# Optimization experiments

Hardware: AMD Instinct MI355X
Metric: run time of the kernel (lower is better)

The kernel has to match this reference:

```python
import jax, jax.numpy as jnp
import numpy as np

B = 131072
# join branch layer dims: 203 -> 175 -> 150 -> 128 -> 80 -> 48
DIMS = [203, 175, 150, 128, 80, 48]

def setup_inputs() -> dict:
    key = jax.random.key(0)
    ks = jax.random.split(key, 11)
    inp = {"x": jax.random.normal(ks[0], (B, DIMS[0]), dtype=jnp.float32)}
    for i in range(5):
        fan_in, fan_out = DIMS[i], DIMS[i + 1]
        bound = 1.0 / np.sqrt(fan_in)
        inp[f"W{i+1}"] = jax.random.uniform(ks[1 + 2 * i], (fan_out, fan_in), minval=-bound, maxval=bound, dtype=jnp.float32)
        inp[f"b{i+1}"] = jax.random.uniform(ks[2 + 2 * i], (fan_out,), minval=-bound, maxval=bound, dtype=jnp.float32)
    return inp

def reference(x, W1, b1, W2, b2, W3, b3, W4, b4, W5, b5):
    # join branch of NodeEmbedding, dropout in eval mode (identity).
    h = jnp.tanh(x @ W1.T + b1)      # [B,175]
    h = jnp.tanh(h @ W2.T + b2)      # [B,150]
    h = jnp.tanh(h @ W3.T + b3)      # [B,128]
    h = jnp.tanh(h @ W4.T + b4)      # [B,80]
    return h @ W5.T + b5             # [B,48], no activation on last layer
```

## Files before the change

kernel.cpp:

```cpp
#include <hip/hip_runtime.h>


typedef short short8 __attribute__((ext_vector_type(8)));
typedef float f32x16 __attribute__((ext_vector_type(16)));
typedef unsigned int uint;
typedef unsigned short ushort;

#define PSTR 116
#define PSTRU (PSTR*2)
#define NTHREADS 384

__device__ __forceinline__ ushort f2bf(float f) {
    uint u = __float_as_uint(f);
    u += 0x7FFFu + ((u >> 16) & 1u);
    return (ushort)(u >> 16);
}
__device__ __forceinline__ float bf2f(ushort h) { return __uint_as_float(((uint)h) << 16); }
__device__ __forceinline__ float fast_tanh(float x) {
    float e = __expf(2.0f * x);
    return 1.0f - 2.0f / (e + 1.0f);
}
__device__ __forceinline__ uint rbf(float v) {
    uint u = __float_as_uint(v);
    return u + 0x7FFFu + ((u >> 16) & 1u);
}

union U4S8 { uint4 u; short8 s; };

__global__ void prep_weights(const float* __restrict__ W1, const float* __restrict__ W2,
                             const float* __restrict__ W3, const float* __restrict__ W4,
                             const float* __restrict__ W5, char* __restrict__ ws)
{
    const int b = blockIdx.x, l = threadIdx.x;
    int layer, local;
    if      (b <  78) { layer = 0; local = b; }
    else if (b < 133) { layer = 1; local = b - 78; }
    else if (b < 173) { layer = 2; local = b - 133; }
    else if (b < 197) { layer = 3; local = b - 173; }
    else              { layer = 4; local = b - 197; }
    const int NTa[5]  = {6, 5, 4, 3, 2};
    const int FINa[5] = {203, 175, 150, 128, 80};
    const int FOa[5]  = {175, 150, 128, 80, 48};
    const float* Wp = (layer == 0) ? W1 : (layer == 1) ? W2 : (layer == 2) ? W3
                    : (layer == 3) ? W4 : W5;
    const int nt = NTa[layer], fin = FINa[layer], fout = FOa[layer];
    const int c = local / nt, t = local % nt;
    const int n  = t * 32 + (l & 31);
    const int kb = c * 16 + (l >> 5) * 8;
    uint hw[4], lw[4];
#pragma unroll
    for (int j = 0; j < 8; ++j) {
        int k = kb + j;
        float v = (n < fout && k < fin) ? Wp[(size_t)n * fin + k] : 0.0f;
        ushort hh = f2bf(v);
        ushort ll = f2bf(v - bf2f(hh));
        if (j & 1) { hw[j >> 1] |= ((uint)hh) << 16; lw[j >> 1] |= ((uint)ll) << 16; }
        else       { hw[j >> 1]  = hh;               lw[j >> 1]  = ll; }
    }
    char* dst = ws + (size_t)b * 2048 + l * 16;
    *(uint4*)dst          = make_uint4(hw[0], hw[1], hw[2], hw[3]);
    *(uint4*)(dst + 1024) = make_uint4(lw[0], lw[1], lw[2], lw[3]);
}

template<int KC, int NT, int FOUT, int PADN, bool ACT, bool LAST>
__device__ __forceinline__ void run_layer(const char* __restrict__ wsL,
    const float* __restrict__ bias, uint* aH, uint* aL, float* outg,
    int row0, int l, int w, int lx, int lh, int tid)
{
    f32x16 acc;
    {
        float bv = 0.0f;
        if (w < NT) { int n = w * 32 + lx; bv = (n < FOUT) ? bias[n] : 0.0f; }
#pragma unroll
        for (int r = 0; r < 16; ++r) acc[r] = bv;
    }

    if (w < NT) {
        const char* ha = (const char*)aH + lx * (PSTR * 4) + lh * 16;
        const char* la = (const char*)aL + lx * (PSTR * 4) + lh * 16;
#pragma unroll
        for (int c = 0; c < KC; ++c) {
            const uint4* wp = (const uint4*)wsL + (size_t)((c * NT + w) * 2) * 64 + l;
            U4S8 bh, bl, ah, al;
            bh.u = wp[0];
            bl.u = wp[64];
            ah.u = *(const uint4*)(ha + c * 32);
            al.u = *(const uint4*)(la + c * 32);
            acc = __builtin_amdgcn_mfma_f32_32x32x16_bf16(ah.s, bh.s, acc, 0, 0, 0);
            acc = __builtin_amdgcn_mfma_f32_32x32x16_bf16(al.s, bh.s, acc, 0, 0, 0);
            acc = __builtin_amdgcn_mfma_f32_32x32x16_bf16(ah.s, bl.s, acc, 0, 0, 0);
        }
    }
    if (!LAST) __syncthreads();

    if (w < NT) {
        ushort* pH = (ushort*)aH;
        ushort* pL = (ushort*)aL;
#pragma unroll
        for (int r = 0; r < 16; ++r) {
            float vv = acc[r];
            if (ACT) vv = fast_tanh(vv);
            int rowl = (r & 3) + 8 * (r >> 2) + 4 * lh;
            int col  = w * 32 + lx;
            if (LAST) {
                if (col < 48) outg[(size_t)(row0 + rowl) * 48 + col] = vv;
            } else if (col < FOUT) {
                uint r1  = rbf(vv);
                uint hib = r1 & 0xFFFF0000u;
                float lo = vv - __uint_as_float(hib);
                uint r2  = rbf(lo);
                pH[rowl * PSTRU + col] = (ushort)(r1 >> 16);
                pL[rowl * PSTRU + col] = (ushort)(r2 >> 16);
            }
        }
    }
    if (!LAST) {
        if (PADN > 0) {
            ushort* pH = (ushort*)aH;
            ushort* pL = (ushort*)aL;
            for (int idx = tid; idx < 32 * PADN; idx += NTHREADS) {
                int row = idx / PADN, p = idx % PADN;
                pH[row * PSTRU + FOUT + p] = 0;
                pL[row * PSTRU + FOUT + p] = 0;
            }
        }
        __syncthreads();
    }
}

__global__ __launch_bounds__(NTHREADS, 5)
void mlp_mfma(const float* __restrict__ x,
              const float* __restrict__ b1, const float* __restrict__ b2,
              const float* __restrict__ b3, const float* __restrict__ b4,
              const float* __restrict__ b5,
              const char* __restrict__ ws, float* __restrict__ out)
{
    __shared__ __align__(16) uint aH[32 * PSTR];
    __shared__ __align__(16) uint aL[32 * PSTR];

    const int tid = threadIdx.x;
    const int l = tid & 63, w = tid >> 6;
    const int lx = l & 31, lh = l >> 5;
    const int row0 = blockIdx.x * 32;

    {
        ushort* pH = (ushort*)aH;
        ushort* pL = (ushort*)aL;
        for (int e = tid; e < 32 * 208; e += NTHREADS) {
            int row = e / 208, col = e - row * 208;
            float v = (col < 203) ? x[(size_t)(row0 + row) * 203 + col] : 0.0f;
            uint r1  = rbf(v);
            uint hib = r1 & 0xFFFF0000u;
            float lo = v - __uint_as_float(hib);
            uint r2  = rbf(lo);
            pH[row * PSTRU + col] = (ushort)(r1 >> 16);
            pL[row * PSTRU + col] = (ushort)(r2 >> 16);
        }
    }
    __syncthreads();

    run_layer<13, 6, 175,  1, true,  false>(ws,              b1, aH, aL, nullptr, row0, l, w, lx, lh, tid);
    run_layer<11, 5, 150, 10, true,  false>(ws +  78 * 2048, b2, aH, aL, nullptr, row0, l, w, lx, lh, tid);
    run_layer<10, 4, 128,  0, true,  false>(ws + 133 * 2048, b3, aH, aL, nullptr, row0, l, w, lx, lh, tid);
    run_layer< 8, 3,  80,  0, true,  false>(ws + 173 * 2048, b4, aH, aL, nullptr, row0, l, w, lx, lh, tid);
    run_layer< 5, 2,  48,  0, false, true >(ws + 197 * 2048, b5, aH, aL, out,     row0, l, w, lx, lh, tid);
}

extern "C" void kernel_launch(void* const* d_in, const int* in_sizes, int n_in,
                              void* d_out, int out_size, void* d_ws, size_t ws_size,
                              hipStream_t stream) {
    (void)in_sizes; (void)n_in; (void)ws_size; (void)out_size;
    const float* x  = (const float*)d_in[0];
    const float* W1 = (const float*)d_in[1];
    const float* b1 = (const float*)d_in[2];
    const float* W2 = (const float*)d_in[3];
    const float* b2 = (const float*)d_in[4];
    const float* W3 = (const float*)d_in[5];
    const float* b3 = (const float*)d_in[6];
    const float* W4 = (const float*)d_in[7];
    const float* b4 = (const float*)d_in[8];
    const float* W5 = (const float*)d_in[9];
    const float* b5 = (const float*)d_in[10];
    float* out = (float*)d_out;
    char* ws = (char*)d_ws;

    hipLaunchKernelGGL(prep_weights, dim3(207), dim3(64), 0, stream,
                       W1, W2, W3, W4, W5, ws);
    hipLaunchKernelGGL(mlp_mfma, dim3(131072 / 32), dim3(NTHREADS), 0, stream,
                       x, b1, b2, b3, b4, b5, ws, out);
}
```

Before: 311.9 us.

## Double-buffer MFMA operand loads and use packed bf16 conversion instructions

Software-pipelines the MFMA inner loop so the weight and activation fragments for the next K chunk load while the current chunk's MFMAs run. Replaces the manual round-to-bf16 bit arithmetic with the hardware v_cvt_pk_bf16_f32 instruction, processing two values at a time in both the input staging and the per-layer epilogue. Swaps the tanh division for a hardware reciprocal. This adds register pressure under a 5-wave launch bound, and the approximate reciprocal slightly changes numerics.

```diff
diff --git a/kernel.cpp b/kernel.cpp
--- a/kernel.cpp
+++ b/kernel.cpp
@@ -18,11 +18,13 @@
 __device__ __forceinline__ float bf2f(ushort h) { return __uint_as_float(((uint)h) << 16); }
 __device__ __forceinline__ float fast_tanh(float x) {
     float e = __expf(2.0f * x);
-    return 1.0f - 2.0f / (e + 1.0f);
-}
-__device__ __forceinline__ uint rbf(float v) {
-    uint u = __float_as_uint(v);
-    return u + 0x7FFFu + ((u >> 16) & 1u);
+    float t = __builtin_amdgcn_rcpf(e + 1.0f);
+    return fmaf(-2.0f, t, 1.0f);
+}
+__device__ __forceinline__ uint cvt_pk_bf16(float s0, float s1) {
+    uint r;
+    asm("v_cvt_pk_bf16_f32 %0, %1, %2" : "=v"(r) : "v"(s0), "v"(s1));
+    return r;
 }
 
 union U4S8 { uint4 u; short8 s; };
@@ -78,14 +80,28 @@
     if (w < NT) {
         const char* ha = (const char*)aH + lx * (PSTR * 4) + lh * 16;
         const char* la = (const char*)aL + lx * (PSTR * 4) + lh * 16;
+        const uint4* wsb = (const uint4*)wsL + (size_t)(w * 2) * 64 + l;
+
+        U4S8 bhA, blA, ahA, alA, bhB, blB, ahB, alB;
+        bhA.u = wsb[0];
+        blA.u = wsb[64];
+        ahA.u = *(const uint4*)(ha);
+        alA.u = *(const uint4*)(la);
+
 #pragma unroll
         for (int c = 0; c < KC; ++c) {
-            const uint4* wp = (const uint4*)wsL + (size_t)((c * NT + w) * 2) * 64 + l;
-            U4S8 bh, bl, ah, al;
-            bh.u = wp[0];
-            bl.u = wp[64];
-            ah.u = *(const uint4*)(ha + c * 32);
-            al.u = *(const uint4*)(la + c * 32);
+            const bool ev = ((c & 1) == 0);
+            U4S8& bh = ev ? bhA : bhB;  U4S8& bl = ev ? blA : blB;
+            U4S8& ah = ev ? ahA : ahB;  U4S8& al = ev ? alA : alB;
+            if (c + 1 < KC) {
+                U4S8& nbh = ev ? bhB : bhA;  U4S8& nbl = ev ? blB : blA;
+                U4S8& nah = ev ? ahB : ahA;  U4S8& nal = ev ? alB : alA;
+                const uint4* wpn = wsb + (size_t)((c + 1) * NT * 2) * 64;
+                nbh.u = wpn[0];
+                nbl.u = wpn[64];
+                nah.u = *(const uint4*)(ha + (c + 1) * 32);
+                nal.u = *(const uint4*)(la + (c + 1) * 32);
+            }
             acc = __builtin_amdgcn_mfma_f32_32x32x16_bf16(ah.s, bh.s, acc, 0, 0, 0);
             acc = __builtin_amdgcn_mfma_f32_32x32x16_bf16(al.s, bh.s, acc, 0, 0, 0);
             acc = __builtin_amdgcn_mfma_f32_32x32x16_bf16(ah.s, bl.s, acc, 0, 0, 0);
@@ -96,21 +112,27 @@
     if (w < NT) {
         ushort* pH = (ushort*)aH;
         ushort* pL = (ushort*)aL;
-#pragma unroll
-        for (int r = 0; r < 16; ++r) {
-            float vv = acc[r];
-            if (ACT) vv = fast_tanh(vv);
-            int rowl = (r & 3) + 8 * (r >> 2) + 4 * lh;
-            int col  = w * 32 + lx;
+        const int col = w * 32 + lx;
+#pragma unroll
+        for (int i = 0; i < 8; ++i) {
+            float v0 = acc[2 * i], v1 = acc[2 * i + 1];
+            if (ACT) { v0 = fast_tanh(v0); v1 = fast_tanh(v1); }
+            const int r0 = 2 * i;
+            const int rowl = (r0 & 3) + 8 * (r0 >> 2) + 4 * lh;
             if (LAST) {
-                if (col < 48) outg[(size_t)(row0 + rowl) * 48 + col] = vv;
+                if (col < 48) {
+                    outg[(size_t)(row0 + rowl) * 48 + col]     = v0;
+                    outg[(size_t)(row0 + rowl + 1) * 48 + col] = v1;
+                }
             } else if (col < FOUT) {
-                uint r1  = rbf(vv);
-                uint hib = r1 & 0xFFFF0000u;
-                float lo = vv - __uint_as_float(hib);
-                uint r2  = rbf(lo);
-                pH[rowl * PSTRU + col] = (ushort)(r1 >> 16);
-                pL[rowl * PSTRU + col] = (ushort)(r2 >> 16);
+                uint chi = cvt_pk_bf16(v0, v1);
+                float h0 = __uint_as_float(chi << 16);
+                float h1 = __uint_as_float(chi & 0xFFFF0000u);
+                uint clo = cvt_pk_bf16(v0 - h0, v1 - h1);
+                pH[rowl * PSTRU + col]       = (ushort)chi;
+                pH[(rowl + 1) * PSTRU + col] = (ushort)(chi >> 16);
+                pL[rowl * PSTRU + col]       = (ushort)clo;
+                pL[(rowl + 1) * PSTRU + col] = (ushort)(clo >> 16);
             }
         }
     }
@@ -143,19 +165,18 @@
     const int lx = l & 31, lh = l >> 5;
     const int row0 = blockIdx.x * 32;
 
-    {
-        ushort* pH = (ushort*)aH;
-        ushort* pL = (ushort*)aL;
-        for (int e = tid; e < 32 * 208; e += NTHREADS) {
-            int row = e / 208, col = e - row * 208;
-            float v = (col < 203) ? x[(size_t)(row0 + row) * 203 + col] : 0.0f;
-            uint r1  = rbf(v);
-            uint hib = r1 & 0xFFFF0000u;
-            float lo = v - __uint_as_float(hib);
-            uint r2  = rbf(lo);
-            pH[row * PSTRU + col] = (ushort)(r1 >> 16);
-            pL[row * PSTRU + col] = (ushort)(r2 >> 16);
-        }
+    for (int e = tid; e < 32 * 104; e += NTHREADS) {
+        int row = e / 104, dcol = e - row * 104;
+        int col = dcol * 2;
+        const float* xp = x + (size_t)(row0 + row) * 203;
+        float v0 = (col < 203) ? xp[col] : 0.0f;
+        float v1 = (col + 1 < 203) ? xp[col + 1] : 0.0f;
+        uint chi = cvt_pk_bf16(v0, v1);
+        float h0 = __uint_as_float(chi << 16);
+        float h1 = __uint_as_float(chi & 0xFFFF0000u);
+        uint clo = cvt_pk_bf16(v0 - h0, v1 - h1);
+        aH[row * PSTR + dcol] = chi;
+        aL[row * PSTR + dcol] = clo;
     }
     __syncthreads();
 
```

New measurement: 280.9 us. 1.11x faster.
